# Kernel tuning notes

Hardware: AMD Instinct MI355X
Metric: run time of the kernel (lower is better)

## Reference

```python
import jax, jax.numpy as jnp
import numpy as np

H, W, C = 80, 80, 64
R = 1.0  # rbf bandwidth (init kwarg r)


def setup_inputs() -> dict:
    key = jax.random.key(0)
    X = jax.random.normal(key, (H, W, C), dtype=jnp.float32)
    return {"X": X}


def reference(X):
    Hh, Ww, Cc = X.shape
    N = Hh * Ww

    # ---- coordinate similarity Ad (vectorized form of the O(N^2) loop) ----
    gr, gc = jnp.meshgrid(jnp.arange(Hh, dtype=X.dtype),
                          jnp.arange(Ww, dtype=X.dtype), indexing='ij')
    rf = gr.reshape(N)  # row coordinate i // W
    cf = gc.reshape(N)  # col coordinate i % W
    # squared euclidean distance between pixel coordinates, [N, N]
    d2 = (rf[:, None] - rf[None, :]) ** 2 + (cf[:, None] - cf[None, :]) ** 2
    Ad = jnp.exp(-d2 / (2.0 * R * R))
    # the python loop only fills i != j, so the diagonal stays 0
    Ad = Ad * (1.0 - jnp.eye(N, dtype=Ad.dtype))
    Ad = Ad / jnp.sum(Ad, axis=-1, keepdims=True)

    # ---- feature similarity As ----
    nodes = X.reshape(N, Cc)                      # [N, C]
    As = jax.nn.softmax(nodes @ nodes.T, axis=-1)  # [N, N], row softmax
    avg = jnp.mean(As, axis=-1, keepdims=True)     # per-row mean
    As = jnp.where(As < avg, jnp.zeros((), As.dtype), As)
    return Ad, As
```

## Files before the change

kernel.cpp:

```cpp
#include <hip/hip_runtime.h>

#define HH 80
#define NN 6400
#define CC 64
#define THR (1.0f / 6400.0f)

typedef _Float16 f16x8 __attribute__((ext_vector_type(8)));
typedef float float4v __attribute__((ext_vector_type(4)));

__global__ __launch_bounds__(256) void prep_kernel(
    const float* __restrict__ X,
    _Float16* __restrict__ Xhi, _Float16* __restrict__ Xlo,
    float* __restrict__ norms, float* __restrict__ denom,
    int* __restrict__ nmax)
{
    const int id = blockIdx.x * 256 + threadIdx.x;
    const float x = X[id];
    const _Float16 h = (_Float16)x;
    const float lo = x - (float)h;
    Xhi[id] = h;
    Xlo[id] = (_Float16)lo;

    float s = x * x;
#pragma unroll
    for (int m = 1; m < 64; m <<= 1) s += __shfl_xor(s, m, 64);
    const int lane = threadIdx.x & 63;
    if (lane == 0) {
        const int row = id >> 6;
        norms[row] = s;
        atomicMax(nmax, __float_as_int(s));
    }
    if (id < NN) denom[id] = 0.f;
}

__global__ __launch_bounds__(256) void pass1_kernel(
    const _Float16* __restrict__ Xhi, const _Float16* __restrict__ Xlo,
    const float* __restrict__ norms, const int* __restrict__ nmaxp,
    float* __restrict__ denom)
{
    const int tid = threadIdx.x;
    const int wave = tid >> 6, lane = tid & 63;
    const int q = lane >> 4, n16 = lane & 15;
    const int i0 = blockIdx.x * 256 + wave * 64;
    const int j0 = blockIdx.y * 256;
    const float nmax = __int_as_float(*nmaxp);

    f16x8 Ah[4][2], Al[4][2];
#pragma unroll
    for (int rt = 0; rt < 4; rt++) {
        const int row = i0 + rt * 16 + n16;
#pragma unroll
        for (int c = 0; c < 2; c++) {
            const int off = row * CC + c * 32 + q * 8;
            Ah[rt][c] = *(const f16x8*)(Xhi + off);
            Al[rt][c] = *(const f16x8*)(Xlo + off);
        }
    }
    float mh[4][4];
#pragma unroll
    for (int rt = 0; rt < 4; rt++)
#pragma unroll
        for (int r = 0; r < 4; r++)
            mh[rt][r] = sqrtf(norms[i0 + rt * 16 + q * 4 + r] * nmax);

    float cs[4][4];
#pragma unroll
    for (int rt = 0; rt < 4; rt++)
#pragma unroll
        for (int r = 0; r < 4; r++) cs[rt][r] = 0.f;

    for (int ct = 0; ct < 16; ct++) {
        const int col = j0 + ct * 16 + n16;
        f16x8 Bh[2], Bl[2];
#pragma unroll
        for (int c = 0; c < 2; c++) {
            const int off = col * CC + c * 32 + q * 8;
            Bh[c] = *(const f16x8*)(Xhi + off);
            Bl[c] = *(const f16x8*)(Xlo + off);
        }
#pragma unroll
        for (int rt = 0; rt < 4; rt++) {
            float4v acc = {0.f, 0.f, 0.f, 0.f};
#pragma unroll
            for (int c = 0; c < 2; c++) {
                acc = __builtin_amdgcn_mfma_f32_16x16x32_f16(Al[rt][c], Bh[c], acc, 0, 0, 0);
                acc = __builtin_amdgcn_mfma_f32_16x16x32_f16(Ah[rt][c], Bl[c], acc, 0, 0, 0);
                acc = __builtin_amdgcn_mfma_f32_16x16x32_f16(Ah[rt][c], Bh[c], acc, 0, 0, 0);
            }
#pragma unroll
            for (int r = 0; r < 4; r++)
                cs[rt][r] += __expf(acc[r] - mh[rt][r]);
        }
    }
#pragma unroll
    for (int rt = 0; rt < 4; rt++)
#pragma unroll
        for (int r = 0; r < 4; r++) {
            float v = cs[rt][r];
            v += __shfl_xor(v, 1, 64);
            v += __shfl_xor(v, 2, 64);
            v += __shfl_xor(v, 4, 64);
            v += __shfl_xor(v, 8, 64);
            if (n16 == 0)
                atomicAdd(&denom[i0 + rt * 16 + q * 4 + r], v);
        }
}

__global__ __launch_bounds__(256) void pass2_kernel(
    const _Float16* __restrict__ Xhi, const _Float16* __restrict__ Xlo,
    const float* __restrict__ norms, const int* __restrict__ nmaxp,
    const float* __restrict__ denom,
    float* __restrict__ Ad, float* __restrict__ As)
{
    __shared__ float Stab[HH];
    __shared__ float sMh[256], sRden[256], sRec[256];
    __shared__ int   sRC[256];
    const int tid = threadIdx.x;
    const int i0 = blockIdx.x * 256;
    const int j0 = blockIdx.y * 64;

    const int wave = tid >> 6, lane = tid & 63;
    const int q = lane >> 4, n16 = lane & 15;
    const int iw = i0 + wave * 64;
    const int jb = j0 + 4 * n16;

    f16x8 Ah[4][2], Al[4][2];
#pragma unroll
    for (int rt = 0; rt < 4; rt++) {
        const int row = iw + rt * 16 + n16;
#pragma unroll
        for (int c = 0; c < 2; c++) {
            const int off = row * CC + c * 32 + q * 8;
            Ah[rt][c] = *(const f16x8*)(Xhi + off);
            Al[rt][c] = *(const f16x8*)(Xlo + off);
        }
    }

    if (tid < HH) {
        float s = 0.f;
        for (int k = 0; k < HH; k++) {
            const float d = (float)(tid - k);
            s += __expf(-0.5f * d * d);
        }
        Stab[tid] = s;
    }
    __syncthreads();
    {
        const int i = i0 + tid;
        const float nmax = __int_as_float(*nmaxp);
        sMh[tid] = sqrtf(norms[i] * nmax);
        sRden[tid] = 1.0f / denom[i];
        const int r = i / HH, c = i - r * HH;
        sRec[tid] = 1.0f / (Stab[r] * Stab[c] - 1.0f);
        sRC[tid] = (r << 8) | c;
    }
    __syncthreads();

    float4v acc[4][4];
#pragma unroll
    for (int rt = 0; rt < 4; rt++)
#pragma unroll
        for (int ct = 0; ct < 4; ct++)
            acc[rt][ct] = (float4v){0.f, 0.f, 0.f, 0.f};

#pragma unroll
    for (int ct = 0; ct < 4; ct++) {
        const int col = jb + ct;
        f16x8 Bh[2], Bl[2];
#pragma unroll
        for (int c = 0; c < 2; c++) {
            const int off = col * CC + c * 32 + q * 8;
            Bh[c] = *(const f16x8*)(Xhi + off);
            Bl[c] = *(const f16x8*)(Xlo + off);
        }
#pragma unroll
        for (int rt = 0; rt < 4; rt++) {
#pragma unroll
            for (int c = 0; c < 2; c++) {
                acc[rt][ct] = __builtin_amdgcn_mfma_f32_16x16x32_f16(Al[rt][c], Bh[c], acc[rt][ct], 0, 0, 0);
                acc[rt][ct] = __builtin_amdgcn_mfma_f32_16x16x32_f16(Ah[rt][c], Bl[c], acc[rt][ct], 0, 0, 0);
                acc[rt][ct] = __builtin_amdgcn_mfma_f32_16x16x32_f16(Ah[rt][c], Bh[c], acc[rt][ct], 0, 0, 0);
            }
        }
    }

    int rj[4], cj[4];
#pragma unroll
    for (int ct = 0; ct < 4; ct++) {
        const int j = jb + ct;
        rj[ct] = j / HH;
        cj[ct] = j - rj[ct] * HH;
    }
#pragma unroll
    for (int rt = 0; rt < 4; rt++) {
#pragma unroll
        for (int r = 0; r < 4; r++) {
            const int il = wave * 64 + rt * 16 + q * 4 + r;
            const int i = i0 + il;
            const float mhv = sMh[il], rden = sRden[il], rec = sRec[il];
            const int rc = sRC[il];
            const int ri = rc >> 8, ci = rc & 255;
            float4v as4, ad4;
#pragma unroll
            for (int ct = 0; ct < 4; ct++) {
                float e = __expf(acc[rt][ct][r] - mhv) * rden;
                if (e < THR) e = 0.f;
                as4[ct] = e;
                const int dr = ri - rj[ct], dc = ci - cj[ct];
                const float d2 = (float)(dr * dr + dc * dc);
                float ad = __expf(-0.5f * d2) * rec;
                if (i == jb + ct) ad = 0.f;
                ad4[ct] = ad;
            }
            __builtin_nontemporal_store(as4, (float4v*)(As + (size_t)i * NN + jb));
            __builtin_nontemporal_store(ad4, (float4v*)(Ad + (size_t)i * NN + jb));
        }
    }
}

extern "C" void kernel_launch(void* const* d_in, const int* in_sizes, int n_in,
                              void* d_out, int out_size, void* d_ws, size_t ws_size,
                              hipStream_t stream) {
    const float* X = (const float*)d_in[0];
    float* Ad = (float*)d_out;
    float* As = Ad + (size_t)NN * NN;

    char* w = (char*)d_ws;
    _Float16* Xhi = (_Float16*)(w);
    _Float16* Xlo = (_Float16*)(w + 819200);
    float* norms  = (float*)(w + 1638400);
    float* denom  = (float*)(w + 1664000);
    int*   nmax   = (int*)(w + 1689600);

    prep_kernel<<<dim3((NN * CC) / 256), dim3(256), 0, stream>>>(
        X, Xhi, Xlo, norms, denom, nmax);
    pass1_kernel<<<dim3(25, 25), dim3(256), 0, stream>>>(
        Xhi, Xlo, norms, nmax, denom);
    pass2_kernel<<<dim3(25, 100), dim3(256), 0, stream>>>(
        Xhi, Xlo, norms, nmax, denom, Ad, As);
}
```

Measured before the change: 445.4 us.

## Widen pass2 column tiles, vectorize prep, closed-form Stab, plain stores

Pass2 blocks now cover 256 columns by looping four 64-column subtiles, which amortises per-block setup and A-fragment loads over more work, and the grid shrinks to 625 blocks. The per-block Stab exp-sum loop and its sync are replaced by a closed-form lookup. The prep kernel processes four elements per thread and reduces the norm max per block before issuing a single atomic, cutting atomic contention. Output stores switch from nontemporal to regular stores, which changes cache behaviour on the large writes. Fewer blocks risk lower latency hiding.

```diff
diff --git a/kernel.cpp b/kernel.cpp
--- a/kernel.cpp
+++ b/kernel.cpp
@@ -6,7 +6,20 @@
 #define THR (1.0f / 6400.0f)
 
 typedef _Float16 f16x8 __attribute__((ext_vector_type(8)));
+typedef _Float16 f16x4 __attribute__((ext_vector_type(4)));
 typedef float float4v __attribute__((ext_vector_type(4)));
+
+__device__ __forceinline__ float stab_of(int t) {
+    const int m = min(t, 79 - t);
+    float v = 2.5066282880428827f;
+    if      (m == 0) v = 1.7533141440214413f;
+    else if (m == 1) v = 2.3598448037340748f;
+    else if (m == 2) v = 2.4951800869706875f;
+    else if (m == 3) v = 2.5062890835089298f;
+    else if (m == 4) v = 2.5066245461368322f;
+    else if (m == 5) v = 2.5066282727900043f;
+    return v;
+}
 
 __global__ __launch_bounds__(256) void prep_kernel(
     const float* __restrict__ X,
@@ -14,23 +27,40 @@
     float* __restrict__ norms, float* __restrict__ denom,
     int* __restrict__ nmax)
 {
-    const int id = blockIdx.x * 256 + threadIdx.x;
-    const float x = X[id];
-    const _Float16 h = (_Float16)x;
-    const float lo = x - (float)h;
-    Xhi[id] = h;
-    Xlo[id] = (_Float16)lo;
-
-    float s = x * x;
-#pragma unroll
-    for (int m = 1; m < 64; m <<= 1) s += __shfl_xor(s, m, 64);
+    __shared__ float sWmax[4];
+    const int t = blockIdx.x * 256 + threadIdx.x;
+    const float4v x = *(const float4v*)(X + 4 * (size_t)t);
+    f16x4 h, l;
+    float s = 0.f;
+#pragma unroll
+    for (int e = 0; e < 4; e++) {
+        const float xe = x[e];
+        const _Float16 he = (_Float16)xe;
+        h[e] = he;
+        l[e] = (_Float16)(xe - (float)he);
+        s += xe * xe;
+    }
+    *(f16x4*)(Xhi + 4 * (size_t)t) = h;
+    *(f16x4*)(Xlo + 4 * (size_t)t) = l;
+
+    s += __shfl_xor(s, 1, 64);
+    s += __shfl_xor(s, 2, 64);
+    s += __shfl_xor(s, 4, 64);
+    s += __shfl_xor(s, 8, 64);
     const int lane = threadIdx.x & 63;
-    if (lane == 0) {
-        const int row = id >> 6;
-        norms[row] = s;
-        atomicMax(nmax, __float_as_int(s));
-    }
-    if (id < NN) denom[id] = 0.f;
+    if ((lane & 15) == 0) norms[t >> 4] = s;
+
+    float m = s;
+    m = fmaxf(m, __shfl_xor(m, 16, 64));
+    m = fmaxf(m, __shfl_xor(m, 32, 64));
+    if (lane == 0) sWmax[threadIdx.x >> 6] = m;
+    __syncthreads();
+    if (threadIdx.x == 0) {
+        const float bm = fmaxf(fmaxf(sWmax[0], sWmax[1]),
+                               fmaxf(sWmax[2], sWmax[3]));
+        atomicMax(nmax, __float_as_int(bm));
+    }
+    if (t < NN) denom[t] = 0.f;
 }
 
 __global__ __launch_bounds__(256) void pass1_kernel(
@@ -112,17 +142,15 @@
     const float* __restrict__ denom,
     float* __restrict__ Ad, float* __restrict__ As)
 {
-    __shared__ float Stab[HH];
     __shared__ float sMh[256], sRden[256], sRec[256];
     __shared__ int   sRC[256];
     const int tid = threadIdx.x;
     const int i0 = blockIdx.x * 256;
-    const int j0 = blockIdx.y * 64;
+    const int j0 = blockIdx.y * 256;
 
     const int wave = tid >> 6, lane = tid & 63;
     const int q = lane >> 4, n16 = lane & 15;
     const int iw = i0 + wave * 64;
-    const int jb = j0 + 4 * n16;
 
     f16x8 Ah[4][2], Al[4][2];
 #pragma unroll
@@ -136,84 +164,79 @@
         }
     }
 
-    if (tid < HH) {
-        float s = 0.f;
-        for (int k = 0; k < HH; k++) {
-            const float d = (float)(tid - k);
-            s += __expf(-0.5f * d * d);
-        }
-        Stab[tid] = s;
-    }
-    __syncthreads();
     {
         const int i = i0 + tid;
         const float nmax = __int_as_float(*nmaxp);
         sMh[tid] = sqrtf(norms[i] * nmax);
         sRden[tid] = 1.0f / denom[i];
         const int r = i / HH, c = i - r * HH;
-        sRec[tid] = 1.0f / (Stab[r] * Stab[c] - 1.0f);
+        sRec[tid] = 1.0f / (stab_of(r) * stab_of(c) - 1.0f);
         sRC[tid] = (r << 8) | c;
     }
     __syncthreads();
 
-    float4v acc[4][4];
-#pragma unroll
-    for (int rt = 0; rt < 4; rt++)
-#pragma unroll
-        for (int ct = 0; ct < 4; ct++)
-            acc[rt][ct] = (float4v){0.f, 0.f, 0.f, 0.f};
-
-#pragma unroll
-    for (int ct = 0; ct < 4; ct++) {
-        const int col = jb + ct;
-        f16x8 Bh[2], Bl[2];
-#pragma unroll
-        for (int c = 0; c < 2; c++) {
-            const int off = col * CC + c * 32 + q * 8;
-            Bh[c] = *(const f16x8*)(Xhi + off);
-            Bl[c] = *(const f16x8*)(Xlo + off);
+    for (int jt = 0; jt < 4; jt++) {
+        const int jb = j0 + jt * 64 + 4 * n16;
+
+        float4v acc[4][4];
+#pragma unroll
+        for (int rt = 0; rt < 4; rt++)
+#pragma unroll
+            for (int ct = 0; ct < 4; ct++)
+                acc[rt][ct] = (float4v){0.f, 0.f, 0.f, 0.f};
+
+#pragma unroll
+        for (int ct = 0; ct < 4; ct++) {
+            const int col = jb + ct;
+            f16x8 Bh[2], Bl[2];
+#pragma unroll
+            for (int c = 0; c < 2; c++) {
+                const int off = col * CC + c * 32 + q * 8;
+                Bh[c] = *(const f16x8*)(Xhi + off);
+                Bl[c] = *(const f16x8*)(Xlo + off);
+            }
+#pragma unroll
+            for (int rt = 0; rt < 4; rt++) {
+#pragma unroll
+                for (int c = 0; c < 2; c++) {
+                    acc[rt][ct] = __builtin_amdgcn_mfma_f32_16x16x32_f16(Al[rt][c], Bh[c], acc[rt][ct], 0, 0, 0);
+                    acc[rt][ct] = __builtin_amdgcn_mfma_f32_16x16x32_f16(Ah[rt][c], Bl[c], acc[rt][ct], 0, 0, 0);
+                    acc[rt][ct] = __builtin_amdgcn_mfma_f32_16x16x32_f16(Ah[rt][c], Bh[c], acc[rt][ct], 0, 0, 0);
+                }
+            }
+        }
+
+        int rj[4], cj[4];
+#pragma unroll
+        for (int ct = 0; ct < 4; ct++) {
+            const int j = jb + ct;
+            rj[ct] = j / HH;
+            cj[ct] = j - rj[ct] * HH;
         }
 #pragma unroll
         for (int rt = 0; rt < 4; rt++) {
 #pragma unroll
-            for (int c = 0; c < 2; c++) {
-                acc[rt][ct] = __builtin_amdgcn_mfma_f32_16x16x32_f16(Al[rt][c], Bh[c], acc[rt][ct], 0, 0, 0);
-                acc[rt][ct] = __builtin_amdgcn_mfma_f32_16x16x32_f16(Ah[rt][c], Bl[c], acc[rt][ct], 0, 0, 0);
-                acc[rt][ct] = __builtin_amdgcn_mfma_f32_16x16x32_f16(Ah[rt][c], Bh[c], acc[rt][ct], 0, 0, 0);
-            }
-        }
-    }
-
-    int rj[4], cj[4];
-#pragma unroll
-    for (int ct = 0; ct < 4; ct++) {
-        const int j = jb + ct;
-        rj[ct] = j / HH;
-        cj[ct] = j - rj[ct] * HH;
-    }
-#pragma unroll
-    for (int rt = 0; rt < 4; rt++) {
-#pragma unroll
-        for (int r = 0; r < 4; r++) {
-            const int il = wave * 64 + rt * 16 + q * 4 + r;
-            const int i = i0 + il;
-            const float mhv = sMh[il], rden = sRden[il], rec = sRec[il];
-            const int rc = sRC[il];
-            const int ri = rc >> 8, ci = rc & 255;
-            float4v as4, ad4;
-#pragma unroll
-            for (int ct = 0; ct < 4; ct++) {
-                float e = __expf(acc[rt][ct][r] - mhv) * rden;
-                if (e < THR) e = 0.f;
-                as4[ct] = e;
-                const int dr = ri - rj[ct], dc = ci - cj[ct];
-                const float d2 = (float)(dr * dr + dc * dc);
-                float ad = __expf(-0.5f * d2) * rec;
-                if (i == jb + ct) ad = 0.f;
-                ad4[ct] = ad;
-            }
-            __builtin_nontemporal_store(as4, (float4v*)(As + (size_t)i * NN + jb));
-            __builtin_nontemporal_store(ad4, (float4v*)(Ad + (size_t)i * NN + jb));
+            for (int r = 0; r < 4; r++) {
+                const int il = wave * 64 + rt * 16 + q * 4 + r;
+                const int i = i0 + il;
+                const float mhv = sMh[il], rden = sRden[il], rec = sRec[il];
+                const int rc = sRC[il];
+                const int ri = rc >> 8, ci = rc & 255;
+                float4v as4, ad4;
+#pragma unroll
+                for (int ct = 0; ct < 4; ct++) {
+                    float e = __expf(acc[rt][ct][r] - mhv) * rden;
+                    if (e < THR) e = 0.f;
+                    as4[ct] = e;
+                    const int dr = ri - rj[ct], dc = ci - cj[ct];
+                    const float d2 = (float)(dr * dr + dc * dc);
+                    float ad = __expf(-0.5f * d2) * rec;
+                    if (i == jb + ct) ad = 0.f;
+                    ad4[ct] = ad;
+                }
+                *(float4v*)(As + (size_t)i * NN + jb) = as4;
+                *(float4v*)(Ad + (size_t)i * NN + jb) = ad4;
+            }
         }
     }
 }
@@ -232,10 +255,10 @@
     float* denom  = (float*)(w + 1664000);
     int*   nmax   = (int*)(w + 1689600);
 
-    prep_kernel<<<dim3((NN * CC) / 256), dim3(256), 0, stream>>>(
+    prep_kernel<<<dim3((NN * CC) / 1024), dim3(256), 0, stream>>>(
         X, Xhi, Xlo, norms, denom, nmax);
     pass1_kernel<<<dim3(25, 25), dim3(256), 0, stream>>>(
         Xhi, Xlo, norms, nmax, denom);
-    pass2_kernel<<<dim3(25, 100), dim3(256), 0, stream>>>(
+    pass2_kernel<<<dim3(25, 25), dim3(256), 0, stream>>>(
         Xhi, Xlo, norms, nmax, denom, Ad, As);
 }
```

New measurement: 381.0 us. 14.5% less time.
